# Kernel optimization log

Hardware: AMD Instinct MI355X
Metric: run time of the kernel (lower is better)

## Reference

```python
import jax, jax.numpy as jnp
import numpy as np

C, H, L, P = 256, 8, 4, 4   # embed_dim, num_heads, num_levels, num_points
B, N = 2, 16384             # batch, total queries
SHAPES = [(64, 64), (128, 128), (256, 256), (512, 512)]  # last = base (finest)


def setup_inputs() -> dict:
    key = jax.random.key(0)
    ks = jax.random.split(key, 16)
    d = {}
    d["query"] = jax.random.normal(ks[0], (N, C), jnp.float32)
    d["query_offsets"] = jnp.array([0, N // 2], jnp.int32)
    base_h, base_w = SHAPES[-1]
    # un-normalized reference points in finest-level pixel coords, kept away from edges
    d["reference_points"] = (
        jax.random.uniform(ks[1], (N, 2), jnp.float32)
        * jnp.array([base_h - 16, base_w - 16], jnp.float32) + 8.0
    )
    for l, (h, w) in enumerate(SHAPES):
        d[f"value{l}"] = jax.random.normal(ks[2 + l], (B, h, w, C), jnp.float32) * 0.1
    d["W_off"] = jax.random.normal(ks[6], (C, H * L * P * 2), jnp.float32) * 0.01
    d["b_off"] = jax.random.normal(ks[7], (H * L * P * 2,), jnp.float32) * 2.0
    d["W_attn"] = jax.random.normal(ks[8], (C, H * L * P), jnp.float32) * 0.02
    d["b_attn"] = jnp.zeros((H * L * P,), jnp.float32)
    d["W_val"] = jax.random.normal(ks[9], (C, C), jnp.float32) * (1.0 / np.sqrt(C))
    d["b_val"] = jnp.zeros((C,), jnp.float32)
    d["W_out"] = jax.random.normal(ks[10], (C, C), jnp.float32) * (1.0 / np.sqrt(C))
    d["b_out"] = jnp.zeros((C,), jnp.float32)
    return d


def _bilinear_sample(v, loc, batch_id):
    """v: [B,h,w,H,dh] per-head feature map; loc: [N,H,P,2] (i,j) pixel coords;
    batch_id: [N]. Returns [N,H,P,dh]. Mirrors sparse_interp: shift by 0.5,
    clamp_min 0, floor, frac weights, max-index clamp."""
    h, w = v.shape[1], v.shape[2]
    sc = jnp.maximum(loc - 0.5, 0.0)
    i0 = jnp.floor(sc).astype(jnp.int32)
    frac = sc - jnp.floor(sc)
    b = batch_id[:, None, None]                 # [N,1,1]
    hidx = jnp.arange(H)[None, :, None]         # [1,H,1]

    def g(di, dj):
        ii = jnp.clip(i0[..., 0] + di, 0, h - 1)
        jj = jnp.clip(i0[..., 1] + dj, 0, w - 1)
        return v[b, ii, jj, hidx]               # [N,H,P,dh]

    dw = frac[..., 0:1]  # down weight
    rw = frac[..., 1:2]  # right weight
    uw, lw = 1.0 - dw, 1.0 - rw
    return uw * lw * g(0, 0) + uw * rw * g(0, 1) + dw * lw * g(1, 0) + dw * rw * g(1, 1)


def reference(query, query_offsets, reference_points, value0, value1, value2, value3,
              W_off, b_off, W_attn, b_attn, W_val, b_val, W_out, b_out):
    values = [value0, value1, value2, value3]
    n = query.shape[0]
    dh = C // H
    # sampling offsets and attention weights from query
    off = (query @ W_off + b_off).reshape(n, H, L, P, 2)
    attn = jax.nn.softmax((query @ W_attn + b_attn).reshape(n, H, L * P), axis=-1)
    attn = attn.reshape(n, H, L, P)
    base = jnp.asarray(values[-1].shape[1:3], jnp.float32)
    # which batch element each query belongs to
    batch_id = jnp.searchsorted(query_offsets, jnp.arange(n), side="right") - 1
    sampled = []
    for l, v in enumerate(values):
        hl, wl = v.shape[1], v.shape[2]
        scaler = jnp.array([hl, wl], jnp.float32) / base
        loc = (reference_points[:, None, None, :] + off[:, :, l]) * scaler  # [N,H,P,2]
        # value_proj: per-pixel 1x1 linear, then split heads
        vp = (v @ W_val + b_val).reshape(v.shape[0], hl, wl, H, dh)
        sampled.append(_bilinear_sample(vp, loc, batch_id))
    sampled = jnp.stack(sampled, axis=2)        # [N,H,L,P,dh]
    out = (sampled * attn[..., None]).sum(axis=(2, 3)).reshape(n, C)
    return out @ W_out + b_out
```

## Files before the change

### kernel.cpp

```cpp
#include <hip/hip_runtime.h>


typedef float f32x4 __attribute__((ext_vector_type(4)));
typedef _Float16 f16;
typedef f16 f16x8 __attribute__((ext_vector_type(8)));
typedef f16 f16x4 __attribute__((ext_vector_type(4)));

template<int M>
__global__ __launch_bounds__(M)
void gemm_rb(const float* __restrict__ X, const float* __restrict__ W,
             const float* __restrict__ bias, float* __restrict__ Y) {
    __shared__ float xt[32 * 256];
    const int tid = threadIdx.x;
    const long row0 = (long)blockIdx.x * 32;
    const float4* src = (const float4*)(X + row0 * 256);
    float4* dst4 = (float4*)xt;
    for (int i = tid; i < 32 * 64; i += M) dst4[i] = src[i];
    __syncthreads();

    constexpr int CG = M / 4;
    const int cg = tid % CG, qg = tid / CG;
    const int c0 = cg * 4, q0 = qg * 8;

    f32x4 acc[8];
#pragma unroll
    for (int qi = 0; qi < 8; ++qi) acc[qi] = (f32x4){0.f, 0.f, 0.f, 0.f};

    for (int k4 = 0; k4 < 64; ++k4) {
        f32x4 w[4];
#pragma unroll
        for (int r = 0; r < 4; ++r)
            w[r] = *(const f32x4*)&W[(size_t)(k4 * 4 + r) * M + c0];
        f32x4 xv[8];
#pragma unroll
        for (int qi = 0; qi < 8; ++qi)
            xv[qi] = *(const f32x4*)&xt[(q0 + qi) * 256 + k4 * 4];
#pragma unroll
        for (int qi = 0; qi < 8; ++qi) {
            f32x4 a = acc[qi];
            const f32x4 x = xv[qi];
            a.x = fmaf(x.x, w[0].x, a.x); a.y = fmaf(x.x, w[0].y, a.y);
            a.z = fmaf(x.x, w[0].z, a.z); a.w = fmaf(x.x, w[0].w, a.w);
            a.x = fmaf(x.y, w[1].x, a.x); a.y = fmaf(x.y, w[1].y, a.y);
            a.z = fmaf(x.y, w[1].z, a.z); a.w = fmaf(x.y, w[1].w, a.w);
            a.x = fmaf(x.z, w[2].x, a.x); a.y = fmaf(x.z, w[2].y, a.y);
            a.z = fmaf(x.z, w[2].z, a.z); a.w = fmaf(x.z, w[2].w, a.w);
            a.x = fmaf(x.w, w[3].x, a.x); a.y = fmaf(x.w, w[3].y, a.y);
            a.z = fmaf(x.w, w[3].z, a.z); a.w = fmaf(x.w, w[3].w, a.w);
            acc[qi] = a;
        }
    }

    const f32x4 bv = *(const f32x4*)&bias[c0];
#pragma unroll
    for (int qi = 0; qi < 8; ++qi) {
        f32x4 o = acc[qi];
        o.x += bv.x; o.y += bv.y; o.z += bv.z; o.w += bv.w;
        *(f32x4*)&Y[(size_t)(row0 + q0 + qi) * M + c0] = o;
    }
}

#define NBINS 4096

__device__ __forceinline__ int bin_of(float ri, float rj) {
    int bi = (int)ri >> 3, bj = (int)rj >> 3;
    bi = min(63, max(0, bi)); bj = min(63, max(0, bj));
    return bi * 64 + bj;
}

__global__ void bin_hist(const float* __restrict__ refp, int* __restrict__ hist, int N) {
    const int n = blockIdx.x * blockDim.x + threadIdx.x;
    if (n < N) atomicAdd(&hist[bin_of(refp[2 * n], refp[2 * n + 1])], 1);
}

__global__ __launch_bounds__(256)
void bin_scan(const int* __restrict__ hist, int* __restrict__ binptr) {
    __shared__ int part[256];
    const int t = threadIdx.x;
    int vals[16], excl[16], run = 0;
#pragma unroll
    for (int i = 0; i < 16; ++i) { vals[i] = hist[t * 16 + i]; }
#pragma unroll
    for (int i = 0; i < 16; ++i) { excl[i] = run; run += vals[i]; }
    part[t] = run;
    __syncthreads();
    int off = 0;
    for (int i = 0; i < t; ++i) off += part[i];
#pragma unroll
    for (int i = 0; i < 16; ++i) binptr[t * 16 + i] = off + excl[i];
}

__global__ void bin_scatter(const float* __restrict__ refp, int* __restrict__ binptr,
                            int* __restrict__ perm, int N) {
    const int n = blockIdx.x * blockDim.x + threadIdx.x;
    if (n < N) {
        const int b = bin_of(refp[2 * n], refp[2 * n + 1]);
        const int pos = atomicAdd(&binptr[b], 1);
        perm[pos] = n;
    }
}

__global__ __launch_bounds__(256)
void prep_wvF(const float* __restrict__ W, f16* __restrict__ wvF) {
    const int k = blockIdx.x, n = threadIdx.x;
    const int ks = k >> 5, kg = (k >> 3) & 3, j = k & 7;
    const int tile = n >> 4, l15 = n & 15;
    const int lane = (kg << 4) | l15;
    wvF[((size_t)(ks * 16 + tile) * 512) + lane * 8 + j] = (f16)W[(size_t)k * 256 + n];
}

__global__ __launch_bounds__(256)
void proj_val_all(const float* __restrict__ v0, const float* __restrict__ v1,
                  const float* __restrict__ v2, const float* __restrict__ v3,
                  const f16* __restrict__ wvF, const float* __restrict__ bval,
                  f16* __restrict__ vp0, f16* __restrict__ vp1,
                  f16* __restrict__ vp2, f16* __restrict__ vp3) {
    __shared__ f16 At[32][264];
    const int tid = threadIdx.x;

    const int bid = blockIdx.x;
    const float* V; f16* VP; long px0;
    if (bid < 256)        { V = v0; VP = vp0; px0 = (long)bid * 32; }
    else if (bid < 1280)  { V = v1; VP = vp1; px0 = (long)(bid - 256) * 32; }
    else if (bid < 5376)  { V = v2; VP = vp2; px0 = (long)(bid - 1280) * 32; }
    else                  { V = v3; VP = vp3; px0 = (long)(bid - 5376) * 32; }

    {
        const int wv_ = tid >> 6, ln_ = tid & 63;
#pragma unroll
        for (int i = 0; i < 8; ++i) {
            const int px = wv_ + i * 4;
            const float4 v4 = *(const float4*)(V + (px0 + px) * 256 + ln_ * 4);
            f16x4 h4 = {(f16)v4.x, (f16)v4.y, (f16)v4.z, (f16)v4.w};
            *(f16x4*)(&At[px][ln_ * 4]) = h4;
        }
    }
    __syncthreads();

    const int wave = tid >> 6, lane = tid & 63;
    const int l15 = lane & 15, kg = lane >> 4;

    f32x4 acc[2][4];
#pragma unroll
    for (int a = 0; a < 2; ++a)
#pragma unroll
        for (int b = 0; b < 4; ++b) acc[a][b] = (f32x4){0.f, 0.f, 0.f, 0.f};

#pragma unroll
    for (int ks = 0; ks < 8; ++ks) {
        f16x8 wf[4];
#pragma unroll
        for (int ct = 0; ct < 4; ++ct)
            wf[ct] = *(const f16x8*)(wvF + ((size_t)(ks * 16 + wave * 4 + ct) * 512) + lane * 8);
        f16x8 vf[2];
#pragma unroll
        for (int pt = 0; pt < 2; ++pt)
            vf[pt] = *(const f16x8*)(&At[pt * 16 + l15][ks * 32 + kg * 8]);
#pragma unroll
        for (int pt = 0; pt < 2; ++pt)
#pragma unroll
            for (int ct = 0; ct < 4; ++ct)
                acc[pt][ct] = __builtin_amdgcn_mfma_f32_16x16x32_f16(wf[ct], vf[pt], acc[pt][ct], 0, 0, 0);
    }

    __syncthreads();

    const int ch0 = wave * 64;
#pragma unroll
    for (int ct = 0; ct < 4; ++ct) {
        const int chb = ch0 + ct * 16 + kg * 4;
        const float4 bv = *(const float4*)(bval + chb);
#pragma unroll
        for (int pt = 0; pt < 2; ++pt) {
            f16x4 o = {(f16)(acc[pt][ct].x + bv.x), (f16)(acc[pt][ct].y + bv.y),
                       (f16)(acc[pt][ct].z + bv.z), (f16)(acc[pt][ct].w + bv.w)};
            *(f16x4*)(&At[pt * 16 + l15][chb]) = o;
        }
    }
    __syncthreads();

    f16* dst = VP + (size_t)px0 * 256;
#pragma unroll
    for (int i = 0; i < 4; ++i) {
        const int e0 = (i * 256 + tid) * 8;
        const int px = e0 >> 8;
        const int ch = e0 & 255;
        *(f16x8*)(dst + e0) = *(const f16x8*)(&At[px][ch]);
    }
}

#define GQPB 8
__global__ __launch_bounds__(256)
void gather_vp(const float* __restrict__ offs_all,
               const float* __restrict__ logits_all,
               const float* __restrict__ refpts,
               const int* __restrict__ qoff, int n_off,
               const int* __restrict__ perm,
               const f16* __restrict__ vp0, const f16* __restrict__ vp1,
               const f16* __restrict__ vp2, const f16* __restrict__ vp3,
               float* __restrict__ val_out) {
    __shared__ float sOff[GQPB][256];
    __shared__ float sAttn[GQPB][128];
    __shared__ int   sQ[GQPB];
    const int tid = threadIdx.x;

    const int bid = blockIdx.x;
    const int cpx = gridDim.x >> 3;
    const int swz = (bid & 7) * cpx + (bid >> 3);
    const int n0p = swz * GQPB;

    if (tid < GQPB) sQ[tid] = perm[n0p + tid];
    __syncthreads();

    {
        const int q = tid >> 5, i = tid & 31;
        const int nq = sQ[q];
        ((f32x4*)sOff[q])[i]      = ((const f32x4*)(offs_all + (size_t)nq * 256))[i];
        ((f32x4*)sOff[q])[i + 32] = ((const f32x4*)(offs_all + (size_t)nq * 256))[i + 32];
        ((f32x4*)sAttn[q])[i]     = ((const f32x4*)(logits_all + (size_t)nq * 128))[i];
    }
    __syncthreads();

    if (tid < GQPB * 8) {
        float* row = &sAttn[tid >> 3][(tid & 7) * 16];
        float m = -1e30f;
#pragma unroll
        for (int i = 0; i < 16; ++i) m = fmaxf(m, row[i]);
        float s = 0.f;
#pragma unroll
        for (int i = 0; i < 16; ++i) { const float e = expf(row[i] - m); row[i] = e; s += e; }
        const float inv = 1.f / s;
#pragma unroll
        for (int i = 0; i < 16; ++i) row[i] *= inv;
    }
    __syncthreads();

    const int q = tid >> 5, h = (tid >> 2) & 7, s = tid & 3;
    const int n = sQ[q];
    int b = 0;
    for (int i = 1; i < n_off; ++i) if (n >= qoff[i]) b = i;
    const float ri = refpts[2 * n], rj = refpts[2 * n + 1];
    const int choff = h * 32 + s * 8;

    float acc[8];
#pragma unroll
    for (int j = 0; j < 8; ++j) acc[j] = 0.f;

#pragma unroll
    for (int l = 0; l < 4; ++l) {
        const int hw = (l == 0 ? 64 : (l == 1 ? 128 : (l == 2 ? 256 : 512)));
        const float sc = (float)hw * (1.0f / 512.0f);
        const f16* vbl = (l == 0 ? vp0 : (l == 1 ? vp1 : (l == 2 ? vp2 : vp3)));
        const f16* __restrict__ vb = vbl + (size_t)b * ((size_t)hw * hw * 256) + choff;

#pragma unroll
        for (int pp = 0; pp < 4; pp += 2) {
            int   o[8];
            float wgt[8];
#pragma unroll
            for (int pq = 0; pq < 2; ++pq) {
                const int p = pp + pq;
                const int oi = ((h * 4 + l) * 4 + p) * 2;
                const float fi = (ri + sOff[q][oi]) * sc;
                const float fj = (rj + sOff[q][oi + 1]) * sc;
                const float a = sAttn[q][(h * 4 + l) * 4 + p];
                const float sci = fmaxf(fi - 0.5f, 0.f);
                const float scj = fmaxf(fj - 0.5f, 0.f);
                const float fl_i = floorf(sci), fl_j = floorf(scj);
                const int i0 = (int)fl_i, j0 = (int)fl_j;
                const float fri = sci - fl_i, frj = scj - fl_j;
                const int i0c = min(i0, hw - 1), i1c = min(i0 + 1, hw - 1);
                const int j0c = min(j0, hw - 1), j1c = min(j0 + 1, hw - 1);
                const float uw = 1.f - fri, lw = 1.f - frj;
                o[pq * 4 + 0] = (i0c * hw + j0c) << 8;
                o[pq * 4 + 1] = (i0c * hw + j1c) << 8;
                o[pq * 4 + 2] = (i1c * hw + j0c) << 8;
                o[pq * 4 + 3] = (i1c * hw + j1c) << 8;
                wgt[pq * 4 + 0] = uw * lw * a;
                wgt[pq * 4 + 1] = uw * frj * a;
                wgt[pq * 4 + 2] = fri * lw * a;
                wgt[pq * 4 + 3] = fri * frj * a;
            }

            f16x8 buf[8];
#pragma unroll
            for (int k = 0; k < 8; ++k)
                buf[k] = *(const f16x8*)(vb + (size_t)o[k]);
            asm volatile("" : "+v"(buf[0]), "+v"(buf[1]), "+v"(buf[2]), "+v"(buf[3]),
                              "+v"(buf[4]), "+v"(buf[5]), "+v"(buf[6]), "+v"(buf[7])
                            :: "memory");
#pragma unroll
            for (int k = 0; k < 8; ++k) {
                const float wv = wgt[k];
#pragma unroll
                for (int j = 0; j < 8; ++j)
                    acc[j] = fmaf(wv, (float)buf[k][j], acc[j]);
            }
        }
    }

    float* op = val_out + (size_t)n * 256 + choff;
    *(f32x4*)op       = (f32x4){acc[0], acc[1], acc[2], acc[3]};
    *(f32x4*)(op + 4) = (f32x4){acc[4], acc[5], acc[6], acc[7]};
}

extern "C" void kernel_launch(void* const* d_in, const int* in_sizes, int n_in,
                              void* d_out, int out_size, void* d_ws, size_t ws_size,
                              hipStream_t stream) {
    const float* query  = (const float*)d_in[0];
    const int*   qoff   = (const int*)d_in[1];
    const float* refp   = (const float*)d_in[2];
    const float* v0     = (const float*)d_in[3];
    const float* v1     = (const float*)d_in[4];
    const float* v2     = (const float*)d_in[5];
    const float* v3     = (const float*)d_in[6];
    const float* W_off  = (const float*)d_in[7];
    const float* b_off  = (const float*)d_in[8];
    const float* W_attn = (const float*)d_in[9];
    const float* b_attn = (const float*)d_in[10];
    const float* W_val  = (const float*)d_in[11];
    const float* b_val  = (const float*)d_in[12];
    const float* W_out  = (const float*)d_in[13];
    const float* b_out  = (const float*)d_in[14];
    float* out = (float*)d_out;

    const int N = in_sizes[0] / 256;
    const int n_off = in_sizes[1];

    float* P1off  = (float*)d_ws;
    float* P1attn = P1off + (size_t)N * 256;
    int*   hist   = (int*)(P1attn + (size_t)N * 128);
    int*   binptr = hist + NBINS;
    int*   perm   = binptr + NBINS;

    const int M0 = 2 * 64 * 64, M1 = 2 * 128 * 128, M2 = 2 * 256 * 256, M3 = 2 * 512 * 512;
    const size_t base_b = (size_t)N * 256 * 4 + (size_t)N * 128 * 4 + (size_t)(2 * NBINS + N) * 4;

    hipMemsetAsync(hist, 0, NBINS * sizeof(int), stream);
    bin_hist<<<(N + 255) / 256, 256, 0, stream>>>(refp, hist, N);
    bin_scan<<<1, 256, 0, stream>>>(hist, binptr);
    bin_scatter<<<(N + 255) / 256, 256, 0, stream>>>(refp, binptr, perm, N);

    gemm_rb<256><<<N / 32, 256, 0, stream>>>(query, W_off, b_off, P1off);
    gemm_rb<128><<<N / 32, 128, 0, stream>>>(query, W_attn, b_attn, P1attn);

    f16* wvF = (f16*)((char*)d_ws + base_b);
    f16* vp0 = wvF + 65536;
    f16* vp1 = vp0 + (size_t)M0 * 256;
    f16* vp2 = vp1 + (size_t)M1 * 256;
    f16* vp3 = vp2 + (size_t)M2 * 256;

    prep_wvF<<<256, 256, 0, stream>>>(W_val, wvF);
    proj_val_all<<<21760, 256, 0, stream>>>(v0, v1, v2, v3, wvF, b_val,
                                            vp0, vp1, vp2, vp3);

    gather_vp<<<N / GQPB, 256, 0, stream>>>(P1off, P1attn, refp, qoff, n_off,
                                            perm, vp0, vp1, vp2, vp3, out);

    gemm_rb<256><<<N / 32, 256, 0, stream>>>(out, W_out, b_out, out);
}
```

Baseline: 558.8 us.

## Fuse offset/attn projections and fold output projection into gather kernel

Merges the two query-projection GEMMs into one 384-thread kernel that computes offset and attention columns together, with padded shared-memory rows to avoid bank conflicts. The final output-projection GEMM is fused into the gather kernel: sampled values are staged in shared memory and each block multiplies its 8 queries by W_out before writing. This removes a launch and the global round-trip of the intermediate values. The trade-off is that the fused output GEMM reuses each W_out load across only 8 queries, so it reads W_out from global far more often than a 32-row tile does.

```diff
diff --git a/kernel.cpp b/kernel.cpp
--- a/kernel.cpp
+++ b/kernel.cpp
@@ -6,21 +6,28 @@
 typedef f16 f16x8 __attribute__((ext_vector_type(8)));
 typedef f16 f16x4 __attribute__((ext_vector_type(4)));
 
-template<int M>
-__global__ __launch_bounds__(M)
-void gemm_rb(const float* __restrict__ X, const float* __restrict__ W,
-             const float* __restrict__ bias, float* __restrict__ Y) {
-    __shared__ float xt[32 * 256];
+__global__ __launch_bounds__(384)
+void gemm_qproj(const float* __restrict__ X,
+                const float* __restrict__ W_off, const float* __restrict__ b_off,
+                const float* __restrict__ W_attn, const float* __restrict__ b_attn,
+                float* __restrict__ Y1, float* __restrict__ Y2) {
+    __shared__ float xt[32 * 260];
     const int tid = threadIdx.x;
     const long row0 = (long)blockIdx.x * 32;
     const float4* src = (const float4*)(X + row0 * 256);
-    float4* dst4 = (float4*)xt;
-    for (int i = tid; i < 32 * 64; i += M) dst4[i] = src[i];
-    __syncthreads();
-
-    constexpr int CG = M / 4;
-    const int cg = tid % CG, qg = tid / CG;
+    for (int i = tid; i < 32 * 64; i += 384) {
+        const int r = i >> 6, c4 = i & 63;
+        *(float4*)(xt + r * 260 + c4 * 4) = src[i];
+    }
+    __syncthreads();
+
+    const int cg = tid % 96, qg = tid / 96;
     const int c0 = cg * 4, q0 = qg * 8;
+    const bool off_part = (c0 < 256);
+    const float* Wp = off_part ? (W_off + c0) : (W_attn + (c0 - 256));
+    const float* bp = off_part ? (b_off + c0) : (b_attn + (c0 - 256));
+    const int ldW = off_part ? 256 : 128;
+    float* Yp = off_part ? (Y1 + c0) : (Y2 + (c0 - 256));
 
     f32x4 acc[8];
 #pragma unroll
@@ -30,11 +37,11 @@
         f32x4 w[4];
 #pragma unroll
         for (int r = 0; r < 4; ++r)
-            w[r] = *(const f32x4*)&W[(size_t)(k4 * 4 + r) * M + c0];
+            w[r] = *(const f32x4*)&Wp[(size_t)(k4 * 4 + r) * ldW];
         f32x4 xv[8];
 #pragma unroll
         for (int qi = 0; qi < 8; ++qi)
-            xv[qi] = *(const f32x4*)&xt[(q0 + qi) * 256 + k4 * 4];
+            xv[qi] = *(const f32x4*)&xt[(q0 + qi) * 260 + k4 * 4];
 #pragma unroll
         for (int qi = 0; qi < 8; ++qi) {
             f32x4 a = acc[qi];
@@ -51,12 +58,12 @@
         }
     }
 
-    const f32x4 bv = *(const f32x4*)&bias[c0];
+    const f32x4 bv = *(const f32x4*)bp;
 #pragma unroll
     for (int qi = 0; qi < 8; ++qi) {
         f32x4 o = acc[qi];
         o.x += bv.x; o.y += bv.y; o.z += bv.z; o.w += bv.w;
-        *(f32x4*)&Y[(size_t)(row0 + q0 + qi) * M + c0] = o;
+        *(f32x4*)&Yp[(size_t)(row0 + q0 + qi) * ldW] = o;
     }
 }
 
@@ -191,14 +198,15 @@
 
 #define GQPB 8
 __global__ __launch_bounds__(256)
-void gather_vp(const float* __restrict__ offs_all,
-               const float* __restrict__ logits_all,
-               const float* __restrict__ refpts,
-               const int* __restrict__ qoff, int n_off,
-               const int* __restrict__ perm,
-               const f16* __restrict__ vp0, const f16* __restrict__ vp1,
-               const f16* __restrict__ vp2, const f16* __restrict__ vp3,
-               float* __restrict__ val_out) {
+void gather_vp_out(const float* __restrict__ offs_all,
+                   const float* __restrict__ logits_all,
+                   const float* __restrict__ refpts,
+                   const int* __restrict__ qoff, int n_off,
+                   const int* __restrict__ perm,
+                   const f16* __restrict__ vp0, const f16* __restrict__ vp1,
+                   const f16* __restrict__ vp2, const f16* __restrict__ vp3,
+                   const float* __restrict__ W_out, const float* __restrict__ b_out,
+                   float* __restrict__ out) {
     __shared__ float sOff[GQPB][256];
     __shared__ float sAttn[GQPB][128];
     __shared__ int   sQ[GQPB];
@@ -299,9 +307,39 @@
         }
     }
 
-    float* op = val_out + (size_t)n * 256 + choff;
-    *(f32x4*)op       = (f32x4){acc[0], acc[1], acc[2], acc[3]};
-    *(f32x4*)(op + 4) = (f32x4){acc[4], acc[5], acc[6], acc[7]};
+    __syncthreads();
+    float* sVal = (float*)sOff;
+    {
+        float* vp = sVal + q * 256 + choff;
+        *(f32x4*)vp       = (f32x4){acc[0], acc[1], acc[2], acc[3]};
+        *(f32x4*)(vp + 4) = (f32x4){acc[4], acc[5], acc[6], acc[7]};
+    }
+    __syncthreads();
+
+    const int c2 = tid;
+    float so[GQPB];
+#pragma unroll
+    for (int qq = 0; qq < GQPB; ++qq) so[qq] = 0.f;
+    for (int k4 = 0; k4 < 64; ++k4) {
+        const float w0 = W_out[(k4 * 4 + 0) * 256 + c2];
+        const float w1 = W_out[(k4 * 4 + 1) * 256 + c2];
+        const float w2 = W_out[(k4 * 4 + 2) * 256 + c2];
+        const float w3 = W_out[(k4 * 4 + 3) * 256 + c2];
+#pragma unroll
+        for (int qq = 0; qq < GQPB; ++qq) {
+            const f32x4 av = *(const f32x4*)(sVal + qq * 256 + k4 * 4);
+            float t = so[qq];
+            t = fmaf(av.x, w0, t);
+            t = fmaf(av.y, w1, t);
+            t = fmaf(av.z, w2, t);
+            t = fmaf(av.w, w3, t);
+            so[qq] = t;
+        }
+    }
+    const float bo = b_out[c2];
+#pragma unroll
+    for (int qq = 0; qq < GQPB; ++qq)
+        out[(size_t)sQ[qq] * 256 + c2] = so[qq] + bo;
 }
 
 extern "C" void kernel_launch(void* const* d_in, const int* in_sizes, int n_in,
@@ -341,8 +379,8 @@
     bin_scan<<<1, 256, 0, stream>>>(hist, binptr);
     bin_scatter<<<(N + 255) / 256, 256, 0, stream>>>(refp, binptr, perm, N);
 
-    gemm_rb<256><<<N / 32, 256, 0, stream>>>(query, W_off, b_off, P1off);
-    gemm_rb<128><<<N / 32, 128, 0, stream>>>(query, W_attn, b_attn, P1attn);
+    gemm_qproj<<<N / 32, 384, 0, stream>>>(query, W_off, b_off, W_attn, b_attn,
+                                           P1off, P1attn);
 
     f16* wvF = (f16*)((char*)d_ws + base_b);
     f16* vp0 = wvF + 65536;
@@ -354,8 +392,7 @@
     proj_val_all<<<21760, 256, 0, stream>>>(v0, v1, v2, v3, wvF, b_val,
                                             vp0, vp1, vp2, vp3);
 
-    gather_vp<<<N / GQPB, 256, 0, stream>>>(P1off, P1attn, refp, qoff, n_off,
-                                            perm, vp0, vp1, vp2, vp3, out);
-
-    gemm_rb<256><<<N / 32, 256, 0, stream>>>(out, W_out, b_out, out);
-}
+    gather_vp_out<<<N / GQPB, 256, 0, stream>>>(P1off, P1attn, refp, qoff, n_off,
+                                                perm, vp0, vp1, vp2, vp3,
+                                                W_out, b_out, out);
+}
```

Measured after the change: 578.9 us. 1.04x slower.
